# Performance work log

Measured on AMD Instinct MI355X. Metric: run time of the kernel, lower is better.

Reference implementation:

```python
import jax, jax.numpy as jnp
import numpy as np

N_LAYERS = 12
N_CH = 256
N_IN = 4
KS = 3
SPECT_CH = 640


def conv1d(x, w, b, dilation):
    # x: [B, T, Cin], w: [K, Cin, Cout] (WIO), SAME padding, given dilation
    y = jax.lax.conv_general_dilated(
        x, w, window_strides=(1,), padding='SAME',
        rhs_dilation=(dilation,), dimension_numbers=('NWC', 'WIO', 'NWC'))
    return y + b


def setup_inputs() -> dict:
    key = jax.random.key(0)
    ks = jax.random.split(key, 16)
    s = 0.02
    inp = {}
    inp['audio'] = jax.random.normal(ks[0], (8, 4096, N_IN), dtype=jnp.float32)
    inp['spect'] = jax.random.normal(ks[1], (8, 4096, SPECT_CH), dtype=jnp.float32)
    # start 1x1 conv: [Cin, Cout]
    inp['w_start'] = jax.random.normal(ks[2], (N_IN, N_CH), dtype=jnp.float32) * s
    inp['b_start'] = jnp.zeros((N_CH,), dtype=jnp.float32)
    # dilated in_layers: stacked [L, K, Cin, 2*Cout]
    inp['w_in'] = jax.random.normal(ks[3], (N_LAYERS, KS, N_CH, 2 * N_CH), dtype=jnp.float32) * s
    inp['b_in'] = jnp.zeros((N_LAYERS, 2 * N_CH), dtype=jnp.float32)
    # cond 1x1 convs: stacked [L, SPECT_CH, 2*Cout]
    inp['w_cond'] = jax.random.normal(ks[4], (N_LAYERS, SPECT_CH, 2 * N_CH), dtype=jnp.float32) * s
    inp['b_cond'] = jnp.zeros((N_LAYERS, 2 * N_CH), dtype=jnp.float32)
    # res_skip 1x1 convs: first L-1 have 2*Cout, last has Cout
    inp['w_res'] = jax.random.normal(ks[5], (N_LAYERS - 1, N_CH, 2 * N_CH), dtype=jnp.float32) * s
    inp['b_res'] = jnp.zeros((N_LAYERS - 1, 2 * N_CH), dtype=jnp.float32)
    inp['w_res_last'] = jax.random.normal(ks[6], (N_CH, N_CH), dtype=jnp.float32) * s
    inp['b_res_last'] = jnp.zeros((N_CH,), dtype=jnp.float32)
    # end 1x1 conv (zero-initialized in the original; use small random for a
    # non-degenerate numerical baseline)
    inp['w_end'] = jax.random.normal(ks[7], (N_CH, 2 * N_IN), dtype=jnp.float32) * s
    inp['b_end'] = jnp.zeros((2 * N_IN,), dtype=jnp.float32)
    return inp


def reference(audio, spect, w_start, b_start, w_in, b_in, w_cond, b_cond,
              w_res, b_res, w_res_last, b_res_last, w_end, b_end):
    # start: 1x1 conv == matmul over channels
    started = jnp.einsum('btc,cd->btd', audio, w_start) + b_start  # [B,T,256]
    # precompute all conditioning projections: [L,B,T,512]
    cond_all = jnp.einsum('btc,lcd->lbtd', spect, w_cond) + b_cond[:, None, None, :]
    output = None
    for i in range(N_LAYERS):
        in_l = conv1d(started, w_in[i], b_in[i], 2 ** i)  # [B,T,512]
        acts = in_l + cond_all[i]
        half_tanh = jnp.tanh(acts[..., :N_CH])
        half_sig = jax.nn.sigmoid(acts[..., N_CH:])
        activated = half_tanh * half_sig  # [B,T,256]
        if i < N_LAYERS - 1:
            rs = jnp.einsum('btc,cd->btd', activated, w_res[i]) + b_res[i]
            started = started + rs[..., :N_CH]
            skip = rs[..., N_CH:]
        else:
            skip = jnp.einsum('btc,cd->btd', activated, w_res_last) + b_res_last
        output = skip if output is None else output + skip
    out = jnp.einsum('btc,cd->btd', output, w_end) + b_end  # [B,T,2*N_IN]
    return out
```

## Files before the change

### kernel.cpp

```cpp
#include <hip/hip_runtime.h>
#include <cstdint>

#define PAD 2048
#define KG 1408

typedef float f32x4 __attribute__((ext_vector_type(4)));
typedef __bf16 bf16x8 __attribute__((ext_vector_type(8)));
typedef __bf16 bf16x4 __attribute__((ext_vector_type(4)));

__device__ __forceinline__ void g2l16(const void* g, void* l) {
    __builtin_amdgcn_global_load_lds(
        (__attribute__((address_space(1))) void*)(uintptr_t)g,
        (__attribute__((address_space(3))) void*)(uint32_t)(uintptr_t)l,
        16, 0, 0);
}


__global__ void cvt_bf16_kernel(const float4* __restrict__ src, bf16x4* __restrict__ dst, int n4) {
    int idx = blockIdx.x * 256 + threadIdx.x;
    if (idx < n4) {
        float4 v = src[idx];
        bf16x4 o = {(__bf16)v.x, (__bf16)v.y, (__bf16)v.z, (__bf16)v.w};
        dst[idx] = o;
    }
}

__global__ void init_started_kernel(const float* __restrict__ audio, const float* __restrict__ w_start,
                                    const float* __restrict__ b_start, __bf16* __restrict__ started_pad) {
    int pr = blockIdx.x * 4 + (threadIdx.x >> 6);
    int c0 = (threadIdx.x & 63) * 4;
    int off = pr & 8191;
    bf16x4 o = {(__bf16)0.f, (__bf16)0.f, (__bf16)0.f, (__bf16)0.f};
    if (off >= PAD && off < PAD + 4096) {
        int r = ((pr >> 13) << 12) + (off - PAD);
        float a0 = audio[r * 4 + 0], a1 = audio[r * 4 + 1], a2 = audio[r * 4 + 2], a3 = audio[r * 4 + 3];
        for (int j = 0; j < 4; ++j) {
            int c = c0 + j;
            o[j] = (__bf16)(b_start[c] + a0 * w_start[c] + a1 * w_start[256 + c]
                            + a2 * w_start[512 + c] + a3 * w_start[768 + c]);
        }
    }
    *(bf16x4*)&started_pad[(size_t)pr * 256 + c0] = o;
}

__global__ void transpose_gate(const float* __restrict__ w_in, const float* __restrict__ w_cond,
                               __bf16* __restrict__ Wg) {
    __shared__ float tile[64][65];
    int i = blockIdx.z;
    int k0 = blockIdx.y * 64, n0 = blockIdx.x * 64;
    int tid = threadIdx.x, c = tid & 63, rr = tid >> 6;
    for (int it = 0; it < 16; ++it) {
        int kl = it * 4 + rr;
        int k = k0 + kl;
        int np = n0 + c;
        int phys = ((np >> 4) & 1) * 256 + (np >> 5) * 16 + (np & 15);
        float v;
        if (k < 768) v = w_in[((i * 3 + (k >> 8)) * 256 + (k & 255)) * 512 + phys];
        else         v = w_cond[(i * 640 + (k - 768)) * 512 + phys];
        tile[kl][c] = v;
    }
    __syncthreads();
    for (int it = 0; it < 16; ++it) {
        int nl = it * 4 + rr;
        Wg[(size_t)(i * 512 + n0 + nl) * KG + k0 + c] = (__bf16)tile[c][nl];
    }
}

__global__ void transpose_kn(const float* __restrict__ src, __bf16* __restrict__ dst,
                             int K, int N, int srcLS, int dstLS) {
    __shared__ float tile[64][65];
    int i = blockIdx.z;
    int k0 = blockIdx.y * 64, n0 = blockIdx.x * 64;
    int tid = threadIdx.x, c = tid & 63, rr = tid >> 6;
    const float* s = src + (size_t)i * srcLS;
    __bf16* dp = dst + (size_t)i * dstLS;
    for (int it = 0; it < 16; ++it) {
        int kl = it * 4 + rr;
        tile[kl][c] = s[(k0 + kl) * N + n0 + c];
    }
    __syncthreads();
    for (int it = 0; it < 16; ++it) {
        int nl = it * 4 + rr;
        dp[(size_t)(n0 + nl) * K + k0 + c] = (__bf16)tile[c][nl];
    }
}

__global__ void bias_gate_kernel(const float* __restrict__ b_in, const float* __restrict__ b_cond,
                                 float* __restrict__ bias) {
    int idx = blockIdx.x * 256 + threadIdx.x;
    int i = idx >> 9, np = idx & 511;
    int phys = ((np >> 4) & 1) * 256 + (np >> 5) * 16 + (np & 15);
    bias[idx] = b_in[i * 512 + phys] + b_cond[i * 512 + phys];
}

__global__ void wfold_kernel(const float* __restrict__ w_res, const float* __restrict__ w_res_last,
                             const float* __restrict__ w_end, const float* __restrict__ b_res,
                             const float* __restrict__ b_res_last, const float* __restrict__ b_end,
                             float* __restrict__ wfold, float* __restrict__ outconst) {
    if (blockIdx.x == 96) {
        __shared__ float red[256][8];
        int j = threadIdx.x;
        float bsum = b_res_last[j];
        for (int i = 0; i < 11; ++i) bsum += b_res[i * 512 + 256 + j];
        for (int c = 0; c < 8; ++c) red[j][c] = bsum * w_end[j * 8 + c];
        __syncthreads();
        if (j < 8) {
            float s = b_end[j];
            for (int t = 0; t < 256; ++t) s += red[t][j];
            outconst[j] = s;
        }
        return;
    }
    int idx = blockIdx.x * 256 + threadIdx.x;
    int i = idx >> 11, rem = idx & 2047, k = rem >> 3, c = rem & 7;
    float s = 0.f;
    if (i < 11) {
        const float* wr = w_res + (size_t)(i * 256 + k) * 512 + 256;
        for (int j = 0; j < 256; ++j) s += wr[j] * w_end[j * 8 + c];
    } else {
        const float* wr = w_res_last + k * 256;
        for (int j = 0; j < 256; ++j) s += wr[j] * w_end[j * 8 + c];
    }
    wfold[idx] = s;
}


__global__ __launch_bounds__(256, 2) void gate_kernel(
    const __bf16* __restrict__ started_pad, const __bf16* __restrict__ spect,
    const __bf16* __restrict__ Wg,
    const float* __restrict__ bias,
    __bf16* __restrict__ activated, int d) {
    __shared__ __align__(16) __bf16 SMEM[30720];
    const int tid = threadIdx.x;
    const int m0 = blockIdx.x * 128;
    const int n0 = blockIdx.y * 256;
    const int padbase = ((m0 >> 12) << 13) + PAD + (m0 & 4095);
    const int srow = tid >> 2;
    const int skq = (tid & 3) * 8;
    const int wave = tid >> 6, lane = tid & 63;
    const int wm = (wave >> 1) * 64, wn = (wave & 1) * 128;
    const int quad = lane >> 4, l15 = lane & 15;

    f32x4 acc[4][8];
    for (int i = 0; i < 4; i++)
        for (int j = 0; j < 8; j++) acc[i][j] = f32x4{0.f, 0.f, 0.f, 0.f};

    const __bf16* Bbase = Wg + (n0 + srow) * KG + skq;

    bf16x8 rA[2], rB[4];
    auto loadTile = [&](int kk) {
        const __bf16* gA0;
        int rstride;
        if (kk < 768) {
            int tap = kk >> 8;
            int koff = kk & 255;
            gA0 = started_pad + (padbase + srow + (tap - 1) * d) * 256 + koff + skq;
            rstride = 256;
        } else {
            gA0 = spect + (m0 + srow) * 640 + (kk - 768) + skq;
            rstride = 640;
        }
        rA[0] = *(const bf16x8*)gA0;
        rA[1] = *(const bf16x8*)(gA0 + 64 * rstride);
        const __bf16* gB0 = Bbase + kk;
        rB[0] = *(const bf16x8*)gB0;
        rB[1] = *(const bf16x8*)(gB0 + 64 * KG);
        rB[2] = *(const bf16x8*)(gB0 + 128 * KG);
        rB[3] = *(const bf16x8*)(gB0 + 192 * KG);
    };
    auto stash = [&](int buf) {
        __bf16* Ab = SMEM + buf * 5120;
        __bf16* Bb = SMEM + 10240 + buf * 10240;
        *(bf16x8*)&Ab[srow * 40 + skq] = rA[0];
        *(bf16x8*)&Ab[(64 + srow) * 40 + skq] = rA[1];
        *(bf16x8*)&Bb[srow * 40 + skq] = rB[0];
        *(bf16x8*)&Bb[(64 + srow) * 40 + skq] = rB[1];
        *(bf16x8*)&Bb[(128 + srow) * 40 + skq] = rB[2];
        *(bf16x8*)&Bb[(192 + srow) * 40 + skq] = rB[3];
    };

    loadTile(0);
    stash(0);
    loadTile(32);
    __syncthreads();

    for (int ks = 0; ks < 44; ++ks) {
        const int cur = ks & 1, nxt = cur ^ 1;
        const __bf16* Ab = SMEM + cur * 5120;
        const __bf16* Bb = SMEM + 10240 + cur * 10240;
        bf16x8 a[4], b[8];
        for (int mi = 0; mi < 4; mi++) a[mi] = *(const bf16x8*)&Ab[(wm + mi * 16 + l15) * 40 + quad * 8];
        for (int ni = 0; ni < 8; ni++) b[ni] = *(const bf16x8*)&Bb[(wn + ni * 16 + l15) * 40 + quad * 8];
        if (ks + 1 < 44) stash(nxt);
        if (ks + 2 < 44) loadTile((ks + 2) * 32);
        for (int mi = 0; mi < 4; mi++)
            for (int ni = 0; ni < 8; ni++)
                acc[mi][ni] = __builtin_amdgcn_mfma_f32_16x16x32_bf16(a[mi], b[ni], acc[mi][ni], 0, 0, 0);
        __syncthreads();
    }

    __bf16* tile = SMEM;
    for (int nj = 0; nj < 4; ++nj) {
        int colT = wn + nj * 32 + l15;
        float bt = bias[n0 + colT];
        float bs = bias[n0 + colT + 16];
        int chl = (wn >> 1) + nj * 16 + l15;
        for (int mi = 0; mi < 4; ++mi) {
            for (int reg = 0; reg < 4; ++reg) {
                int row = wm + mi * 16 + quad * 4 + reg;
                float xt = acc[mi][2 * nj][reg] + bt;
                float xs = acc[mi][2 * nj + 1][reg] + bs;
                float th = 2.f / (1.f + __expf(-2.f * xt)) - 1.f;
                float sg = 1.f / (1.f + __expf(-xs));
                tile[row * 132 + chl] = (__bf16)(th * sg);
            }
        }
    }
    __syncthreads();
    int chb = n0 >> 1;
    for (int pass = 0; pass < 8; ++pass) {
        int row = (tid >> 4) + 16 * pass;
        int seg = tid & 15;
        bf16x8 v = *(const bf16x8*)&tile[row * 132 + seg * 8];
        *(bf16x8*)&activated[(m0 + row) * 256 + chb + seg * 8] = v;
    }
}

__global__ __launch_bounds__(256) void res_kernel(
    const __bf16* __restrict__ activated, const __bf16* __restrict__ Wr,
    const float* __restrict__ b_res,
    const float* __restrict__ wfold,
    const float* __restrict__ outconst,
    __bf16* __restrict__ started_pad, float* __restrict__ out, int initOut) {
    __shared__ __align__(16) __bf16 As[128 * 32];
    __shared__ __align__(16) __bf16 Bs[128 * 32];
    __shared__ __align__(16) __bf16 WfB[16 * 264];
    const int tid = threadIdx.x;
    const int m0 = blockIdx.x * 128;
    const int n0 = blockIdx.y * 128;
    const int srow = tid >> 2;
    const int skq = (tid & 3) * 8;
    const int wave = tid >> 6, lane = tid & 63;
    const int wm = (wave >> 1) * 64, wn = (wave & 1) * 64;
    const int quad = lane >> 4, l15 = lane & 15;
    const bool doOut = (blockIdx.y == 0);
    const bool outWave = doOut && (wn == 0);

    f32x4 acc[4][4];
    for (int i = 0; i < 4; i++)
        for (int j = 0; j < 4; j++) acc[i][j] = f32x4{0.f, 0.f, 0.f, 0.f};
    f32x4 acc_o[4];
    for (int i = 0; i < 4; i++) acc_o[i] = f32x4{0.f, 0.f, 0.f, 0.f};

    const __bf16* Abase = activated + (m0 + srow) * 256 + skq;
    const __bf16* Bbase = Wr + (n0 + srow) * 256 + skq;

    if (doOut) {
        for (int t = 0; t < 16; ++t) {
            int e = t * 256 + tid;
            int col = e >> 8, k = e & 255;
            WfB[col * 264 + k] = (col < 8) ? (__bf16)wfold[k * 8 + col] : (__bf16)0.f;
        }
    }

    for (int ks = 0; ks < 8; ++ks) {
        int kk = ks * 32;
        g2l16(Abase + kk, &As[srow * 32 + skq]);
        g2l16(Abase + kk + 64 * 256, &As[(64 + srow) * 32 + skq]);
        g2l16(Bbase + kk, &Bs[srow * 32 + skq]);
        g2l16(Bbase + kk + 64 * 256, &Bs[(64 + srow) * 32 + skq]);
        __syncthreads();
        bf16x8 a[4], b[4];
        for (int mi = 0; mi < 4; mi++) a[mi] = *(const bf16x8*)&As[(wm + mi * 16 + l15) * 32 + quad * 8];
        for (int ni = 0; ni < 4; ni++) b[ni] = *(const bf16x8*)&Bs[(wn + ni * 16 + l15) * 32 + quad * 8];
        for (int mi = 0; mi < 4; mi++)
            for (int ni = 0; ni < 4; ni++)
                acc[mi][ni] = __builtin_amdgcn_mfma_f32_16x16x32_bf16(a[mi], b[ni], acc[mi][ni], 0, 0, 0);
        if (outWave) {
            bf16x8 bx = *(const bf16x8*)&WfB[l15 * 264 + kk + quad * 8];
            for (int mi = 0; mi < 4; mi++)
                acc_o[mi] = __builtin_amdgcn_mfma_f32_16x16x32_bf16(a[mi], bx, acc_o[mi], 0, 0, 0);
        }
        __syncthreads();
    }

    for (int ni = 0; ni < 4; ++ni) {
        int col = n0 + wn + ni * 16 + l15;
        float bcol = b_res[col];
        for (int mi = 0; mi < 4; ++mi) {
            for (int reg = 0; reg < 4; ++reg) {
                int r = m0 + wm + mi * 16 + quad * 4 + reg;
                int pr = ((r >> 12) << 13) + PAD + (r & 4095);
                int idx = pr * 256 + col;
                float f = (float)started_pad[idx] + acc[mi][ni][reg] + bcol;
                started_pad[idx] = (__bf16)f;
            }
        }
    }
    if (outWave && l15 < 8) {
        for (int mi = 0; mi < 4; ++mi) {
            for (int reg = 0; reg < 4; ++reg) {
                int r = m0 + wm + mi * 16 + quad * 4 + reg;
                float base = initOut ? outconst[l15] : out[r * 8 + l15];
                out[r * 8 + l15] = base + acc_o[mi][reg];
            }
        }
    }
}

__global__ __launch_bounds__(256) void outacc_kernel(
    const __bf16* __restrict__ activated, const float* __restrict__ wfold,
    float* __restrict__ out) {
    __shared__ __align__(16) float Wf[2048];
    int tid = threadIdx.x;
    ((float4*)Wf)[tid] = ((const float4*)wfold)[tid];
    ((float4*)Wf)[256 + tid] = ((const float4*)wfold)[256 + tid];
    __syncthreads();
    int row2 = tid >> 1, half = tid & 1;
    int r = blockIdx.x * 128 + row2;
    const bf16x8* ap = (const bf16x8*)(activated + r * 256);
    const float4* wf = (const float4*)Wf;
    float ox = 0.f, oy = 0.f, oz = 0.f, ow = 0.f;
    for (int c8 = 0; c8 < 32; ++c8) {
        bf16x8 av = ap[c8];
        for (int e = 0; e < 8; ++e) {
            float a = (float)av[e];
            float4 w = wf[(c8 * 8 + e) * 2 + half];
            ox += a * w.x; oy += a * w.y; oz += a * w.z; ow += a * w.w;
        }
    }
    float4* op = (float4*)&out[r * 8 + half * 4];
    float4 o = *op;
    o.x += ox; o.y += oy; o.z += oz; o.w += ow;
    *op = o;
}


extern "C" void kernel_launch(void* const* d_in, const int* in_sizes, int n_in,
                              void* d_out, int out_size, void* d_ws, size_t ws_size,
                              hipStream_t stream) {
    const float* audio      = (const float*)d_in[0];
    const float* spect      = (const float*)d_in[1];
    const float* w_start    = (const float*)d_in[2];
    const float* b_start    = (const float*)d_in[3];
    const float* w_in       = (const float*)d_in[4];
    const float* b_in       = (const float*)d_in[5];
    const float* w_cond     = (const float*)d_in[6];
    const float* b_cond     = (const float*)d_in[7];
    const float* w_res      = (const float*)d_in[8];
    const float* b_res      = (const float*)d_in[9];
    const float* w_res_last = (const float*)d_in[10];
    const float* b_res_last = (const float*)d_in[11];
    const float* w_end      = (const float*)d_in[12];
    const float* b_end      = (const float*)d_in[13];
    float* out = (float*)d_out;

    char* ws = (char*)d_ws;
    __bf16* started_pad = (__bf16*)ws; ws += 33554432;
    __bf16* activated   = (__bf16*)ws; ws += 16777216;
    __bf16* spect_bf    = (__bf16*)ws; ws += 41943040;
    __bf16* Wg          = (__bf16*)ws; ws += 17301504;
    __bf16* Wr          = (__bf16*)ws; ws += 1441792;
    float*  wfold       = (float*)ws;  ws += 98304;
    float*  biasg       = (float*)ws;  ws += 24576;
    float*  outconst    = (float*)ws;  ws += 256;

    init_started_kernel<<<dim3(16384), 256, 0, stream>>>(audio, w_start, b_start, started_pad);
    cvt_bf16_kernel<<<dim3(20480), 256, 0, stream>>>((const float4*)spect, (bf16x4*)spect_bf, 5242880);
    transpose_gate<<<dim3(8, 22, 12), 256, 0, stream>>>(w_in, w_cond, Wg);
    transpose_kn<<<dim3(4, 4, 11), 256, 0, stream>>>(w_res, Wr, 256, 512, 256 * 512, 256 * 256);
    bias_gate_kernel<<<dim3(24), 256, 0, stream>>>(b_in, b_cond, biasg);
    wfold_kernel<<<dim3(97), 256, 0, stream>>>(w_res, w_res_last, w_end, b_res, b_res_last, b_end,
                                               wfold, outconst);

    for (int i = 0; i < 12; ++i) {
        gate_kernel<<<dim3(256, 2), 256, 0, stream>>>(
            started_pad, spect_bf, Wg + (size_t)i * 512 * KG, biasg + i * 512, activated, 1 << i);
        if (i < 11) {
            res_kernel<<<dim3(256, 2), 256, 0, stream>>>(
                activated, Wr + (size_t)i * 256 * 256, b_res + i * 512,
                wfold + i * 2048, outconst, started_pad, out, i == 0 ? 1 : 0);
        } else {
            outacc_kernel<<<dim3(256), 256, 0, stream>>>(activated, wfold + 11 * 2048, out);
        }
    }
}
```

Measured before the change: 1.094 ms.

## Restructure gate GEMM with 256x256 tiles, direct global-to-LDS loads and 4-stage pipeline

Rewrites the gated-conv GEMM kernel to use 512-thread blocks computing 256x256 output tiles. Operands now move directly from global memory into LDS through a 4-slot ring with XOR-swizzled layout, replacing the register-staged double buffer. Barriers split each k-step into two MFMA phases with raised wave priority, so loads overlap compute. The aim is more data reuse per tile and better latency hiding, at the cost of 128KB LDS per block, which limits occupancy, and a fragile hand-written vmcnt/barrier schedule.

```diff
diff --git a/kernel.cpp b/kernel.cpp
--- a/kernel.cpp
+++ b/kernel.cpp
@@ -125,89 +125,118 @@
 }
 
 
-__global__ __launch_bounds__(256, 2) void gate_kernel(
+__global__ __launch_bounds__(512, 2) void gate_kernel(
     const __bf16* __restrict__ started_pad, const __bf16* __restrict__ spect,
     const __bf16* __restrict__ Wg,
     const float* __restrict__ bias,
     __bf16* __restrict__ activated, int d) {
-    __shared__ __align__(16) __bf16 SMEM[30720];
+    __shared__ __align__(16) __bf16 SMEM[65536];
     const int tid = threadIdx.x;
-    const int m0 = blockIdx.x * 128;
+    const int m0 = blockIdx.x * 256;
     const int n0 = blockIdx.y * 256;
     const int padbase = ((m0 >> 12) << 13) + PAD + (m0 & 4095);
+    const int wave = tid >> 6, lane = tid & 63;
+    const int wr = wave >> 2, wc = wave & 3;
+    const int quad = lane >> 4, l15 = lane & 15;
+
     const int srow = tid >> 2;
-    const int skq = (tid & 3) * 8;
-    const int wave = tid >> 6, lane = tid & 63;
-    const int wm = (wave >> 1) * 64, wn = (wave & 1) * 128;
-    const int quad = lane >> 4, l15 = lane & 15;
-
-    f32x4 acc[4][8];
-    for (int i = 0; i < 4; i++)
-        for (int j = 0; j < 8; j++) acc[i][j] = f32x4{0.f, 0.f, 0.f, 0.f};
-
-    const __bf16* Bbase = Wg + (n0 + srow) * KG + skq;
-
-    bf16x8 rA[2], rB[4];
-    auto loadTile = [&](int kk) {
-        const __bf16* gA0;
-        int rstride;
-        if (kk < 768) {
-            int tap = kk >> 8;
-            int koff = kk & 255;
-            gA0 = started_pad + (padbase + srow + (tap - 1) * d) * 256 + koff + skq;
-            rstride = 256;
+    const int scw = ((tid & 3) * 8) ^ (((tid >> 3) & 3) << 3);
+
+    f32x4 acc[8][4];
+    #pragma unroll
+    for (int i = 0; i < 8; i++)
+        #pragma unroll
+        for (int j = 0; j < 4; j++) acc[i][j] = f32x4{0.f, 0.f, 0.f, 0.f};
+
+    auto stageA = [&](int kt, int s) {
+        const __bf16* g0;
+        int rs;
+        if (kt < 24) {
+            int tap = kt >> 3;
+            int cb = (kt & 7) * 32;
+            g0 = started_pad + (padbase + (tap - 1) * d) * 256 + cb + scw;
+            rs = 256;
         } else {
-            gA0 = spect + (m0 + srow) * 640 + (kk - 768) + skq;
-            rstride = 640;
-        }
-        rA[0] = *(const bf16x8*)gA0;
-        rA[1] = *(const bf16x8*)(gA0 + 64 * rstride);
-        const __bf16* gB0 = Bbase + kk;
-        rB[0] = *(const bf16x8*)gB0;
-        rB[1] = *(const bf16x8*)(gB0 + 64 * KG);
-        rB[2] = *(const bf16x8*)(gB0 + 128 * KG);
-        rB[3] = *(const bf16x8*)(gB0 + 192 * KG);
+            int cb = (kt - 24) * 32;
+            g0 = spect + (size_t)m0 * 640 + cb + scw;
+            rs = 640;
+        }
+        __bf16* As = SMEM + s * 8192;
+        g2l16(g0 + srow * rs, As + tid * 8);
+        g2l16(g0 + (128 + srow) * rs, As + 4096 + tid * 8);
     };
-    auto stash = [&](int buf) {
-        __bf16* Ab = SMEM + buf * 5120;
-        __bf16* Bb = SMEM + 10240 + buf * 10240;
-        *(bf16x8*)&Ab[srow * 40 + skq] = rA[0];
-        *(bf16x8*)&Ab[(64 + srow) * 40 + skq] = rA[1];
-        *(bf16x8*)&Bb[srow * 40 + skq] = rB[0];
-        *(bf16x8*)&Bb[(64 + srow) * 40 + skq] = rB[1];
-        *(bf16x8*)&Bb[(128 + srow) * 40 + skq] = rB[2];
-        *(bf16x8*)&Bb[(192 + srow) * 40 + skq] = rB[3];
+    auto stageB = [&](int kt, int s) {
+        const __bf16* g0 = Wg + (size_t)(n0 + srow) * KG + kt * 32 + scw;
+        __bf16* Bs = SMEM + 32768 + s * 8192;
+        g2l16(g0, Bs + tid * 8);
+        g2l16(g0 + 128 * KG, Bs + 4096 + tid * 8);
     };
 
-    loadTile(0);
-    stash(0);
-    loadTile(32);
-    __syncthreads();
-
-    for (int ks = 0; ks < 44; ++ks) {
-        const int cur = ks & 1, nxt = cur ^ 1;
-        const __bf16* Ab = SMEM + cur * 5120;
-        const __bf16* Bb = SMEM + 10240 + cur * 10240;
-        bf16x8 a[4], b[8];
-        for (int mi = 0; mi < 4; mi++) a[mi] = *(const bf16x8*)&Ab[(wm + mi * 16 + l15) * 40 + quad * 8];
-        for (int ni = 0; ni < 8; ni++) b[ni] = *(const bf16x8*)&Bb[(wn + ni * 16 + l15) * 40 + quad * 8];
-        if (ks + 1 < 44) stash(nxt);
-        if (ks + 2 < 44) loadTile((ks + 2) * 32);
-        for (int mi = 0; mi < 4; mi++)
-            for (int ni = 0; ni < 8; ni++)
-                acc[mi][ni] = __builtin_amdgcn_mfma_f32_16x16x32_bf16(a[mi], b[ni], acc[mi][ni], 0, 0, 0);
-        __syncthreads();
+    stageA(0, 0); stageB(0, 0);
+    stageA(1, 1); stageB(1, 1);
+    asm volatile("s_waitcnt vmcnt(4)" ::: "memory");
+    __builtin_amdgcn_s_barrier();
+
+    for (int j = 0; j < 44; ++j) {
+        const int s = j & 3;
+        const __bf16* Asl = SMEM + s * 8192;
+        const __bf16* Bsl = SMEM + 32768 + s * 8192;
+
+        bf16x8 b[4];
+        #pragma unroll
+        for (int nf = 0; nf < 4; ++nf) {
+            int br = wc * 64 + nf * 16 + l15;
+            b[nf] = *(const bf16x8*)&Bsl[br * 32 + ((quad * 8) ^ (((br >> 1) & 3) << 3))];
+        }
+        bf16x8 a[4];
+        #pragma unroll
+        for (int f = 0; f < 4; ++f) {
+            int ar = wr * 128 + f * 16 + l15;
+            a[f] = *(const bf16x8*)&Asl[ar * 32 + ((quad * 8) ^ (((ar >> 1) & 3) << 3))];
+        }
+        if (j + 2 < 44) stageA(j + 2, (j + 2) & 3);
+        __builtin_amdgcn_s_barrier();
+        __builtin_amdgcn_s_setprio(1);
+        #pragma unroll
+        for (int f = 0; f < 4; ++f)
+            #pragma unroll
+            for (int nf = 0; nf < 4; ++nf)
+                acc[f][nf] = __builtin_amdgcn_mfma_f32_16x16x32_bf16(a[f], b[nf], acc[f][nf], 0, 0, 0);
+        __builtin_amdgcn_s_setprio(0);
+        __builtin_amdgcn_s_barrier();
+        #pragma unroll
+        for (int f = 0; f < 4; ++f) {
+            int ar = wr * 128 + 64 + f * 16 + l15;
+            a[f] = *(const bf16x8*)&Asl[ar * 32 + ((quad * 8) ^ (((ar >> 1) & 3) << 3))];
+        }
+        if (j + 2 < 44) stageB(j + 2, (j + 2) & 3);
+        if (j + 1 < 44) {
+            if (j + 2 < 44) asm volatile("s_waitcnt vmcnt(4)" ::: "memory");
+            else            asm volatile("s_waitcnt vmcnt(0)" ::: "memory");
+        }
+        __builtin_amdgcn_s_barrier();
+        __builtin_amdgcn_s_setprio(1);
+        #pragma unroll
+        for (int f = 0; f < 4; ++f)
+            #pragma unroll
+            for (int nf = 0; nf < 4; ++nf)
+                acc[4 + f][nf] = __builtin_amdgcn_mfma_f32_16x16x32_bf16(a[f], b[nf], acc[4 + f][nf], 0, 0, 0);
+        __builtin_amdgcn_s_setprio(0);
+        __builtin_amdgcn_s_barrier();
     }
 
     __bf16* tile = SMEM;
-    for (int nj = 0; nj < 4; ++nj) {
-        int colT = wn + nj * 32 + l15;
+    #pragma unroll
+    for (int nj = 0; nj < 2; ++nj) {
+        int colT = wc * 64 + nj * 32 + l15;
         float bt = bias[n0 + colT];
         float bs = bias[n0 + colT + 16];
-        int chl = (wn >> 1) + nj * 16 + l15;
-        for (int mi = 0; mi < 4; ++mi) {
+        int chl = wc * 32 + nj * 16 + l15;
+        #pragma unroll
+        for (int mi = 0; mi < 8; ++mi) {
+            #pragma unroll
             for (int reg = 0; reg < 4; ++reg) {
-                int row = wm + mi * 16 + quad * 4 + reg;
+                int row = wr * 128 + mi * 16 + quad * 4 + reg;
                 float xt = acc[mi][2 * nj][reg] + bt;
                 float xs = acc[mi][2 * nj + 1][reg] + bs;
                 float th = 2.f / (1.f + __expf(-2.f * xt)) - 1.f;
@@ -219,7 +248,7 @@
     __syncthreads();
     int chb = n0 >> 1;
     for (int pass = 0; pass < 8; ++pass) {
-        int row = (tid >> 4) + 16 * pass;
+        int row = (tid >> 4) + 32 * pass;
         int seg = tid & 15;
         bf16x8 v = *(const bf16x8*)&tile[row * 132 + seg * 8];
         *(bf16x8*)&activated[(m0 + row) * 256 + chb + seg * 8] = v;
@@ -374,7 +403,7 @@
                                                wfold, outconst);
 
     for (int i = 0; i < 12; ++i) {
-        gate_kernel<<<dim3(256, 2), 256, 0, stream>>>(
+        gate_kernel<<<dim3(128, 2), 512, 0, stream>>>(
             started_pad, spect_bf, Wg + (size_t)i * 512 * KG, biasg + i * 512, activated, 1 << i);
         if (i < 11) {
             res_kernel<<<dim3(256, 2), 256, 0, stream>>>(
```

Measured after the change: 1.056 ms. 1.04x faster.
